# Kernel tuning notes

Hardware: AMD Instinct MI355X
Metric: run time of the kernel (lower is better)

Reference implementation:

```python
import jax, jax.numpy as jnp
import numpy as np

N, M, D = 32768, 2048, 32


def setup_inputs() -> dict:
    key = jax.random.key(0)
    k1, k2, k3, k4 = jax.random.split(key, 4)
    inputs = jax.random.normal(k1, (N, D), dtype=jnp.float32)
    # matches torch init: abs(10*randn*0.1 + 0.2)
    gamma = jnp.abs(10.0 * jax.random.normal(k2, (M, D, D), dtype=jnp.float32) * 0.1 + 0.2)
    means = jax.random.normal(k3, (M, D), dtype=jnp.float32)
    weights = jax.random.normal(k4, (M,), dtype=jnp.float32)
    return {"inputs": inputs, "gamma": gamma, "means": means, "weights": weights}


def reference(inputs, gamma, means, weights):
    # cov_m = gamma_m @ gamma_m^T  -> symmetric PSD [M, D, D]
    cov = jnp.einsum('mde,mfe->mdf', gamma, gamma)
    # Quadratic form (x - mu)^T C (x - mu) expanded (C symmetric):
    # x^T C_m x via GEMM on flattened outer products: [N, D*D] @ [D*D, M]
    xx = (inputs[:, :, None] * inputs[:, None, :]).reshape(inputs.shape[0], -1)
    quad_x = xx @ cov.reshape(cov.shape[0], -1).T            # [N, M]
    b = jnp.einsum('mde,me->md', cov, means)                 # C_m mu_m, [M, D]
    cross = inputs @ b.T                                     # x^T C_m mu_m, [N, M]
    const = jnp.einsum('md,md->m', b, means)                 # mu^T C mu, [M]
    D_ij = quad_x - 2.0 * cross + const[None, :]             # [N, M]
    out = jnp.exp(-D_ij) @ weights                           # [N]
    return out[:, None]
```

## Files before the change

### kernel.cpp

```cpp
#include <hip/hip_runtime.h>
#include <math.h>


#define NN 32768
#define MM 2048
#define DDIM 32
#define KSYM 576
#define ROWS 128
#define KSTEPS 18
#define SCREEN 120.0f
#define MCAP 2048
#define FCAP 1000000
#define FBLK 64

typedef __attribute__((ext_vector_type(8))) short short8;
typedef __attribute__((ext_vector_type(4))) float floatx4;

__device__ __forceinline__ unsigned int to_bf16(float f) {
  union { float f; unsigned int u; } x; x.f = f;
  return (x.u + 0x7fffu + ((x.u >> 16) & 1u)) >> 16;
}

struct DFTab { unsigned char d[528]; unsigned char f[528]; };
constexpr DFTab make_df() {
  DFTab t{};
  int s = 0;
  for (int d = 0; d < 32; ++d)
    for (int f = d; f < 32; ++f) {
      t.d[s] = (unsigned char)d; t.f[s] = (unsigned char)f; ++s;
    }
  return t;
}
constexpr DFTab DFT = make_df();

__device__ __forceinline__ float slot_val(const float* v, int s) {
  if (s < 528) return v[DFT.d[s]] * v[DFT.f[s]];
  if (s < 560) return v[s - 528];
  if (s < 562) return 1.f;
  return 0.f;
}

__device__ __forceinline__ void slot_df(int s, int* dd, int* ff) {
  int d = 0, b = 0;
  while (b + (DDIM - d) <= s) { b += DDIM - d; ++d; }
  *dd = d; *ff = d + (s - b);
}

__global__ __launch_bounds__(256) void build_b_kernel(
    const float* __restrict__ gamma, const float* __restrict__ means,
    unsigned short* __restrict__ Bm, double* __restrict__ acc,
    unsigned int* __restrict__ mcnt, unsigned int* __restrict__ fcount) {
  __shared__ float G[DDIM][DDIM + 1];
  __shared__ float C[DDIM][DDIM + 1];
  __shared__ float bv[DDIM];
  __shared__ float cc;
  const int m = blockIdx.x;
  const int t = threadIdx.x;
  if (t < 16) acc[m * 16 + t] = 0.0;
  if (t == 16) mcnt[m] = 0u;
  if (m == 0 && t == 17) *fcount = 0u;
  const float* g = gamma + (size_t)m * DDIM * DDIM;
  for (int l = t; l < DDIM * DDIM; l += 256) G[l >> 5][l & 31] = g[l];
  __syncthreads();
  const float* mu = means + m * DDIM;
  for (int l = t; l < DDIM * DDIM; l += 256) {
    int d = l >> 5, f = l & 31;
    float c = 0.f;
#pragma unroll
    for (int e = 0; e < DDIM; ++e) c += G[d][e] * G[f][e];
    C[d][f] = c;
  }
  __syncthreads();
  if (t < DDIM) {
    float b = 0.f;
#pragma unroll
    for (int f = 0; f < DDIM; ++f) b += C[t][f] * mu[f];
    bv[t] = b;
  }
  __syncthreads();
  if (t == 0) {
    float c = 0.f;
#pragma unroll
    for (int d = 0; d < DDIM; ++d) c += bv[d] * mu[d];
    cc = c;
  }
  __syncthreads();
  unsigned short* brow = Bm + (size_t)m * KSYM;
  for (int s = t; s < KSYM; s += 256) {
    float val;
    if (s < 528) {
      int d, f; slot_df(s, &d, &f);
      val = (d == f) ? C[d][d] : 2.f * C[d][f];
    } else if (s < 560) {
      val = -2.f * bv[s - 528];
    } else if (s == 560) {
      val = cc;
    } else if (s == 561) {
      unsigned int hi = to_bf16(cc);
      union { unsigned int u; float f; } xh; xh.u = hi << 16;
      val = cc - xh.f;
    } else {
      val = 0.f;
    }
    brow[s] = (unsigned short)to_bf16(val);
  }
}

__device__ __noinline__ double survivor_contrib(
    int m, const float* __restrict__ gamma, const float* __restrict__ means,
    const float* __restrict__ weights, const float* __restrict__ xrow) {
  const float* mu = means + m * DDIM;
  float v[DDIM];
#pragma unroll
  for (int d = 0; d < DDIM; ++d) v[d] = xrow[d] - mu[d];
  const float* g = gamma + (size_t)m * DDIM * DDIM;
  float Dex = 0.f;
  for (int e = 0; e < DDIM; ++e) {
    float y = 0.f;
#pragma unroll
    for (int d = 0; d < DDIM; ++d) y += g[d * DDIM + e] * v[d];
    Dex += y * y;
  }
  float e2 = -Dex * 1.44269504088896340736f;
  float kf = floorf(e2);
  float mant = exp2f(e2 - kf);
  return ldexp((double)(weights[m] * mant), (int)kf);
}

__global__ __launch_bounds__(512, 1) void screen_kernel(
    const float* __restrict__ x, const unsigned short* __restrict__ Bm,
    unsigned int* __restrict__ mcnt, unsigned short* __restrict__ mlist,
    unsigned int* __restrict__ flist, unsigned int* __restrict__ fcount) {
  extern __shared__ __align__(16) unsigned short As[];
  const int t = threadIdx.x;
  const int i0 = blockIdx.x * ROWS;
  const int lane = t & 63, w = t >> 6;
  const int lrow = lane & 15, quad = lane >> 4;
  const int rot = blockIdx.x & 31;

  {
    const int r = t >> 2, j = t & 3;
    float v[DDIM];
#pragma unroll
    for (int q = 0; q < 8; ++q)
      *(floatx4*)&v[q * 4] = *(const floatx4*)(x + (size_t)(i0 + r) * DDIM + q * 4);
#pragma unroll
    for (int jj = 0; jj < 4; ++jj) {
      if (j == jj) {
#pragma unroll
        for (int cc2 = 0; cc2 < 18; ++cc2) {
          const int c = jj * 18 + cc2;
          unsigned int uu[4];
#pragma unroll
          for (int q = 0; q < 4; ++q) {
            const int s0 = c * 8 + q * 2;
            uu[q] = to_bf16(slot_val(v, s0)) | (to_bf16(slot_val(v, s0 + 1)) << 16);
          }
          const int cs = (c & ~7) | ((c & 7) ^ (r & 7));
          uint4 o; o.x = uu[0]; o.y = uu[1]; o.z = uu[2]; o.w = uu[3];
          *(uint4*)&As[r * KSYM + cs * 8] = o;
        }
      }
    }
  }
  __syncthreads();

#pragma unroll 1
  for (int g = 0; g < 4; ++g) {
    const int mq = ((g * 8 + w) + rot) & 31;
    const int m0 = mq * 64;
    const unsigned short* bb0 = Bm + (size_t)(m0 +  0 + lrow) * KSYM + quad * 8;
    const unsigned short* bb1 = Bm + (size_t)(m0 + 16 + lrow) * KSYM + quad * 8;
    const unsigned short* bb2 = Bm + (size_t)(m0 + 32 + lrow) * KSYM + quad * 8;
    const unsigned short* bb3 = Bm + (size_t)(m0 + 48 + lrow) * KSYM + quad * 8;

    floatx4 acc[8][4] = {};
#pragma unroll
    for (int kk = 0; kk < KSTEPS; ++kk) {
      short8 bf[4];
      bf[0] = *(const short8*)(bb0 + kk * 32);
      bf[1] = *(const short8*)(bb1 + kk * 32);
      bf[2] = *(const short8*)(bb2 + kk * 32);
      bf[3] = *(const short8*)(bb3 + kk * 32);
      short8 af[8];
#pragma unroll
      for (int ti = 0; ti < 8; ++ti) {
        int rr = ti * 16 + lrow;
        int c = kk * 4 + quad;
        int cs = (c & ~7) | ((c & 7) ^ (rr & 7));
        af[ti] = *(const short8*)&As[rr * KSYM + cs * 8];
      }
#pragma unroll
      for (int ti = 0; ti < 8; ++ti)
#pragma unroll
        for (int mj = 0; mj < 4; ++mj)
          acc[ti][mj] = __builtin_amdgcn_mfma_f32_16x16x32_bf16(
              af[ti], bf[mj], acc[ti][mj], 0, 0, 0);
    }

#pragma unroll
    for (int ti = 0; ti < 8; ++ti)
#pragma unroll
      for (int mj = 0; mj < 4; ++mj)
#pragma unroll
        for (int r = 0; r < 4; ++r) {
          float Dt = acc[ti][mj][r];
          if (Dt < SCREEN) {
            int gi = i0 + ti * 16 + quad * 4 + r;
            int gm = m0 + mj * 16 + lrow;
            unsigned int idx = atomicAdd(&mcnt[gm], 1u);
            if (idx < MCAP) {
              mlist[(size_t)gm * MCAP + idx] = (unsigned short)gi;
            } else {
              unsigned int fi = atomicAdd(fcount, 1u);
              if (fi < FCAP)
                flist[fi] = ((unsigned int)gi << 11) | (unsigned int)gm;
            }
          }
        }
  }
}

__global__ __launch_bounds__(256) void survivor2_kernel(
    const unsigned int* __restrict__ mcnt, const unsigned short* __restrict__ mlist,
    const unsigned int* __restrict__ flist, const unsigned int* __restrict__ fcount,
    const float* __restrict__ x, const float* __restrict__ gamma,
    const float* __restrict__ means, const float* __restrict__ weights,
    double* __restrict__ acc_out) {
  const int blk = blockIdx.x;
  const int t = threadIdx.x;
  if (blk >= MM) {
    unsigned int total = *fcount;
    if (total > FCAP) total = FCAP;
    for (unsigned int idx = (blk - MM) * 256 + t; idx < total; idx += FBLK * 256) {
      unsigned int p = flist[idx];
      int gi = (int)(p >> 11), gm = (int)(p & 2047u);
      double c = survivor_contrib(gm, gamma, means, weights, x + (size_t)gi * DDIM);
      atomicAdd(&acc_out[gi], c);
    }
    return;
  }
  __shared__ float Gt[DDIM][DDIM + 1];
  __shared__ float mu[DDIM];
  const int m = blk;
  unsigned int cnt = mcnt[m];
  if (cnt > MCAP) cnt = MCAP;
  if (cnt == 0) return;
  const float* g = gamma + (size_t)m * DDIM * DDIM;
  for (int l = t; l < DDIM * DDIM; l += 256) Gt[l & 31][l >> 5] = g[l];
  if (t < DDIM) mu[t] = means[m * DDIM + t];
  __syncthreads();
  const float wm = weights[m];
  for (unsigned int s = t; s < cnt; s += 256) {
    int gi = mlist[(size_t)m * MCAP + s];
    float v[DDIM];
#pragma unroll
    for (int q = 0; q < 8; ++q) {
      floatx4 xv = *(const floatx4*)(x + (size_t)gi * DDIM + q * 4);
      v[q * 4 + 0] = xv.x - mu[q * 4 + 0];
      v[q * 4 + 1] = xv.y - mu[q * 4 + 1];
      v[q * 4 + 2] = xv.z - mu[q * 4 + 2];
      v[q * 4 + 3] = xv.w - mu[q * 4 + 3];
    }
    float Dex = 0.f;
#pragma unroll
    for (int e = 0; e < DDIM; ++e) {
      float y = 0.f;
#pragma unroll
      for (int d = 0; d < DDIM; ++d) y += Gt[e][d] * v[d];
      Dex += y * y;
    }
    float e2 = -Dex * 1.44269504088896340736f;
    float kf = floorf(e2);
    float mant = exp2f(e2 - kf);
    atomicAdd(&acc_out[gi], ldexp((double)(wm * mant), (int)kf));
  }
}

__global__ __launch_bounds__(256) void finalize_kernel(
    const double* __restrict__ acc, float* __restrict__ out) {
  int i = blockIdx.x * 256 + threadIdx.x;
  out[i] = (float)acc[i];
}

extern "C" void kernel_launch(void* const* d_in, const int* in_sizes, int n_in,
                              void* d_out, int out_size, void* d_ws, size_t ws_size,
                              hipStream_t stream) {
  (void)in_sizes; (void)n_in; (void)out_size;
  const float* x       = (const float*)d_in[0];
  const float* gamma   = (const float*)d_in[1];
  const float* means   = (const float*)d_in[2];
  const float* weights = (const float*)d_in[3];

  char* p = (char*)d_ws;
  double* acc          = (double*)p;            p += (size_t)NN * 8;
  unsigned int* fcount = (unsigned int*)p;      p += 16;
  unsigned int* mcnt   = (unsigned int*)p;      p += (size_t)MM * 4;
  unsigned short* mlist= (unsigned short*)p;    p += (size_t)MM * MCAP * 2;
  unsigned int* flist  = (unsigned int*)p;      p += (size_t)FCAP * 4;
  unsigned short* Bm   = (unsigned short*)p;    p += (size_t)MM * KSYM * 2;
  const size_t needed = (size_t)(p - (char*)d_ws);
  if (ws_size < needed) return;

  (void)hipFuncSetAttribute((const void*)screen_kernel,
                            hipFuncAttributeMaxDynamicSharedMemorySize,
                            ROWS * KSYM * 2);

  hipLaunchKernelGGL(build_b_kernel, dim3(MM), dim3(256), 0, stream,
                     gamma, means, Bm, acc, mcnt, fcount);
  hipLaunchKernelGGL(screen_kernel, dim3(NN / ROWS), dim3(512),
                     ROWS * KSYM * 2, stream,
                     x, Bm, mcnt, mlist, flist, fcount);
  hipLaunchKernelGGL(survivor2_kernel, dim3(MM + FBLK), dim3(256), 0, stream,
                     mcnt, mlist, flist, fcount, x, gamma, means, weights, acc);
  hipLaunchKernelGGL(finalize_kernel, dim3(NN / 256), dim3(256), 0, stream,
                     acc, (float*)d_out);
}
```

Before: 182.8 us.

## Precompute bf16 outer-product A matrix in separate kernel; use 16-wave screen blocks

The expansion of each input row into its symmetric outer-product features moves out of the screen kernel into a new agen_kernel that writes them to a global workspace. The screen kernel now copies its 128-row tile straight into shared memory. Blocks grow to 1024 threads, and each wave computes a 64-row by 64-column tile, so the accumulator array halves and register pressure drops. The cost is an extra kernel launch plus a write and re-read of a 32768x576 bf16 buffer through global memory.

```diff
diff --git a/kernel.cpp b/kernel.cpp
--- a/kernel.cpp
+++ b/kernel.cpp
@@ -106,6 +106,31 @@
   }
 }
 
+__global__ __launch_bounds__(256) void agen_kernel(
+    const float* __restrict__ x, unsigned short* __restrict__ Ag) {
+  const int t = threadIdx.x;
+  const int r = blockIdx.x * 32 + (t >> 3);
+  const int j = t & 7;
+  float v[DDIM];
+#pragma unroll
+  for (int q = 0; q < 8; ++q)
+    *(floatx4*)&v[q * 4] = *(const floatx4*)(x + (size_t)r * DDIM + q * 4);
+  unsigned short* arow = Ag + (size_t)r * KSYM;
+#pragma unroll
+  for (int cc2 = 0; cc2 < 9; ++cc2) {
+    const int c = cc2 * 8 + j;
+    unsigned int uu[4];
+#pragma unroll
+    for (int q = 0; q < 4; ++q) {
+      const int s0 = c * 8 + q * 2;
+      uu[q] = to_bf16(slot_val(v, s0)) | (to_bf16(slot_val(v, s0 + 1)) << 16);
+    }
+    const int cs = (c & ~7) | ((c & 7) ^ (r & 7));
+    uint4 o; o.x = uu[0]; o.y = uu[1]; o.z = uu[2]; o.w = uu[3];
+    *(uint4*)&arow[cs * 8] = o;
+  }
+}
+
 __device__ __noinline__ double survivor_contrib(
     int m, const float* __restrict__ gamma, const float* __restrict__ means,
     const float* __restrict__ weights, const float* __restrict__ xrow) {
@@ -127,8 +152,10 @@
   return ldexp((double)(weights[m] * mant), (int)kf);
 }
 
-__global__ __launch_bounds__(512, 1) void screen_kernel(
-    const float* __restrict__ x, const unsigned short* __restrict__ Bm,
+__global__ __launch_bounds__(1024)
+__attribute__((amdgpu_waves_per_eu(4, 4)))
+void screen_kernel(
+    const unsigned short* __restrict__ Ag, const unsigned short* __restrict__ Bm,
     unsigned int* __restrict__ mcnt, unsigned short* __restrict__ mlist,
     unsigned int* __restrict__ flist, unsigned int* __restrict__ fcount) {
   extern __shared__ __align__(16) unsigned short As[];
@@ -139,42 +166,26 @@
   const int rot = blockIdx.x & 31;
 
   {
-    const int r = t >> 2, j = t & 3;
-    float v[DDIM];
-#pragma unroll
-    for (int q = 0; q < 8; ++q)
-      *(floatx4*)&v[q * 4] = *(const floatx4*)(x + (size_t)(i0 + r) * DDIM + q * 4);
-#pragma unroll
-    for (int jj = 0; jj < 4; ++jj) {
-      if (j == jj) {
-#pragma unroll
-        for (int cc2 = 0; cc2 < 18; ++cc2) {
-          const int c = jj * 18 + cc2;
-          unsigned int uu[4];
-#pragma unroll
-          for (int q = 0; q < 4; ++q) {
-            const int s0 = c * 8 + q * 2;
-            uu[q] = to_bf16(slot_val(v, s0)) | (to_bf16(slot_val(v, s0 + 1)) << 16);
-          }
-          const int cs = (c & ~7) | ((c & 7) ^ (r & 7));
-          uint4 o; o.x = uu[0]; o.y = uu[1]; o.z = uu[2]; o.w = uu[3];
-          *(uint4*)&As[r * KSYM + cs * 8] = o;
-        }
-      }
-    }
+    const uint4* __restrict__ src = (const uint4*)(Ag + (size_t)i0 * KSYM);
+    uint4* __restrict__ dst = (uint4*)As;
+#pragma unroll
+    for (int ofs = 0; ofs < 9; ++ofs)
+      dst[ofs * 1024 + t] = src[ofs * 1024 + t];
   }
   __syncthreads();
 
 #pragma unroll 1
   for (int g = 0; g < 4; ++g) {
-    const int mq = ((g * 8 + w) + rot) & 31;
-    const int m0 = mq * 64;
+    const int task = g * 16 + w;
+    const int rh = task >> 5;
+    const int cg = ((task & 31) + rot) & 31;
+    const int m0 = cg * 64;
     const unsigned short* bb0 = Bm + (size_t)(m0 +  0 + lrow) * KSYM + quad * 8;
     const unsigned short* bb1 = Bm + (size_t)(m0 + 16 + lrow) * KSYM + quad * 8;
     const unsigned short* bb2 = Bm + (size_t)(m0 + 32 + lrow) * KSYM + quad * 8;
     const unsigned short* bb3 = Bm + (size_t)(m0 + 48 + lrow) * KSYM + quad * 8;
 
-    floatx4 acc[8][4] = {};
+    floatx4 acc[4][4] = {};
 #pragma unroll
     for (int kk = 0; kk < KSTEPS; ++kk) {
       short8 bf[4];
@@ -182,31 +193,28 @@
       bf[1] = *(const short8*)(bb1 + kk * 32);
       bf[2] = *(const short8*)(bb2 + kk * 32);
       bf[3] = *(const short8*)(bb3 + kk * 32);
-      short8 af[8];
-#pragma unroll
-      for (int ti = 0; ti < 8; ++ti) {
-        int rr = ti * 16 + lrow;
-        int c = kk * 4 + quad;
-        int cs = (c & ~7) | ((c & 7) ^ (rr & 7));
-        af[ti] = *(const short8*)&As[rr * KSYM + cs * 8];
-      }
-#pragma unroll
-      for (int ti = 0; ti < 8; ++ti)
+#pragma unroll
+      for (int ti = 0; ti < 4; ++ti) {
+        const int rr = rh * 64 + ti * 16 + lrow;
+        const int c = kk * 4 + quad;
+        const int cs = (c & ~7) | ((c & 7) ^ (rr & 7));
+        short8 a = *(const short8*)&As[rr * KSYM + cs * 8];
 #pragma unroll
         for (int mj = 0; mj < 4; ++mj)
           acc[ti][mj] = __builtin_amdgcn_mfma_f32_16x16x32_bf16(
-              af[ti], bf[mj], acc[ti][mj], 0, 0, 0);
-    }
-
-#pragma unroll
-    for (int ti = 0; ti < 8; ++ti)
+              a, bf[mj], acc[ti][mj], 0, 0, 0);
+      }
+    }
+
+#pragma unroll
+    for (int ti = 0; ti < 4; ++ti)
 #pragma unroll
       for (int mj = 0; mj < 4; ++mj)
 #pragma unroll
         for (int r = 0; r < 4; ++r) {
           float Dt = acc[ti][mj][r];
           if (Dt < SCREEN) {
-            int gi = i0 + ti * 16 + quad * 4 + r;
+            int gi = i0 + rh * 64 + ti * 16 + quad * 4 + r;
             int gm = m0 + mj * 16 + lrow;
             unsigned int idx = atomicAdd(&mcnt[gm], 1u);
             if (idx < MCAP) {
@@ -299,6 +307,7 @@
   unsigned short* mlist= (unsigned short*)p;    p += (size_t)MM * MCAP * 2;
   unsigned int* flist  = (unsigned int*)p;      p += (size_t)FCAP * 4;
   unsigned short* Bm   = (unsigned short*)p;    p += (size_t)MM * KSYM * 2;
+  unsigned short* Ag   = (unsigned short*)p;    p += (size_t)NN * KSYM * 2;
   const size_t needed = (size_t)(p - (char*)d_ws);
   if (ws_size < needed) return;
 
@@ -308,9 +317,11 @@
 
   hipLaunchKernelGGL(build_b_kernel, dim3(MM), dim3(256), 0, stream,
                      gamma, means, Bm, acc, mcnt, fcount);
-  hipLaunchKernelGGL(screen_kernel, dim3(NN / ROWS), dim3(512),
+  hipLaunchKernelGGL(agen_kernel, dim3(NN / 32), dim3(256), 0, stream,
+                     x, Ag);
+  hipLaunchKernelGGL(screen_kernel, dim3(NN / ROWS), dim3(1024),
                      ROWS * KSYM * 2, stream,
-                     x, Bm, mcnt, mlist, flist, fcount);
+                     Ag, Bm, mcnt, mlist, flist, fcount);
   hipLaunchKernelGGL(survivor2_kernel, dim3(MM + FBLK), dim3(256), 0, stream,
                      mcnt, mlist, flist, fcount, x, gamma, means, weights, acc);
   hipLaunchKernelGGL(finalize_kernel, dim3(NN / 256), dim3(256), 0, stream,
```

Result: slower. 307.0 us (+67.9%).

## Precompute swizzled bf16 outer-product rows in prep kernel and stream into LDS

Applied to the files above, without the earlier changes.

The per-row symmetric outer-product expansion and bf16 packing moves out of the screen kernel into extra blocks of the prep kernel, which write a pre-swizzled global buffer Ag. The screen kernel now copies that buffer straight into shared memory with wide loads, instead of computing it with a thread layout where only a quarter of the lanes were active at a time. The A-fragment LDS addresses are also precomputed per tile row to cut address arithmetic in the MFMA inner loop. The cost is an extra 36 MB global write and read round trip plus a larger workspace.

```diff
diff --git a/kernel.cpp b/kernel.cpp
--- a/kernel.cpp
+++ b/kernel.cpp
@@ -46,16 +46,41 @@
   *dd = d; *ff = d + (s - b);
 }
 
-__global__ __launch_bounds__(256) void build_b_kernel(
+__global__ __launch_bounds__(256) void prep_kernel(
     const float* __restrict__ gamma, const float* __restrict__ means,
     unsigned short* __restrict__ Bm, double* __restrict__ acc,
-    unsigned int* __restrict__ mcnt, unsigned int* __restrict__ fcount) {
+    unsigned int* __restrict__ mcnt, unsigned int* __restrict__ fcount,
+    const float* __restrict__ x, unsigned short* __restrict__ Ag) {
+  const int t = threadIdx.x;
+  if (blockIdx.x >= MM) {
+    const int blk = blockIdx.x - MM;
+    const int r = blk * 32 + (t >> 3);
+    const int j = t & 7;
+    float v[DDIM];
+#pragma unroll
+    for (int q = 0; q < 8; ++q)
+      *(floatx4*)&v[q * 4] = *(const floatx4*)(x + (size_t)r * DDIM + q * 4);
+    unsigned short* arow = Ag + (size_t)r * KSYM;
+#pragma unroll
+    for (int cc2 = 0; cc2 < 9; ++cc2) {
+      const int c = cc2 * 8 + j;
+      unsigned int uu[4];
+#pragma unroll
+      for (int q = 0; q < 4; ++q) {
+        const int s0 = c * 8 + q * 2;
+        uu[q] = to_bf16(slot_val(v, s0)) | (to_bf16(slot_val(v, s0 + 1)) << 16);
+      }
+      const int cs = (c & ~7) | ((c & 7) ^ (r & 7));
+      uint4 o; o.x = uu[0]; o.y = uu[1]; o.z = uu[2]; o.w = uu[3];
+      *(uint4*)&arow[cs * 8] = o;
+    }
+    return;
+  }
   __shared__ float G[DDIM][DDIM + 1];
   __shared__ float C[DDIM][DDIM + 1];
   __shared__ float bv[DDIM];
   __shared__ float cc;
   const int m = blockIdx.x;
-  const int t = threadIdx.x;
   if (t < 16) acc[m * 16 + t] = 0.0;
   if (t == 16) mcnt[m] = 0u;
   if (m == 0 && t == 17) *fcount = 0u;
@@ -128,7 +153,7 @@
 }
 
 __global__ __launch_bounds__(512, 1) void screen_kernel(
-    const float* __restrict__ x, const unsigned short* __restrict__ Bm,
+    const unsigned short* __restrict__ Ag, const unsigned short* __restrict__ Bm,
     unsigned int* __restrict__ mcnt, unsigned short* __restrict__ mlist,
     unsigned int* __restrict__ flist, unsigned int* __restrict__ fcount) {
   extern __shared__ __align__(16) unsigned short As[];
@@ -139,31 +164,23 @@
   const int rot = blockIdx.x & 31;
 
   {
-    const int r = t >> 2, j = t & 3;
-    float v[DDIM];
-#pragma unroll
-    for (int q = 0; q < 8; ++q)
-      *(floatx4*)&v[q * 4] = *(const floatx4*)(x + (size_t)(i0 + r) * DDIM + q * 4);
-#pragma unroll
-    for (int jj = 0; jj < 4; ++jj) {
-      if (j == jj) {
-#pragma unroll
-        for (int cc2 = 0; cc2 < 18; ++cc2) {
-          const int c = jj * 18 + cc2;
-          unsigned int uu[4];
-#pragma unroll
-          for (int q = 0; q < 4; ++q) {
-            const int s0 = c * 8 + q * 2;
-            uu[q] = to_bf16(slot_val(v, s0)) | (to_bf16(slot_val(v, s0 + 1)) << 16);
-          }
-          const int cs = (c & ~7) | ((c & 7) ^ (r & 7));
-          uint4 o; o.x = uu[0]; o.y = uu[1]; o.z = uu[2]; o.w = uu[3];
-          *(uint4*)&As[r * KSYM + cs * 8] = o;
-        }
-      }
-    }
-  }
-  __syncthreads();
+    const uint4* __restrict__ src = (const uint4*)(Ag + (size_t)i0 * KSYM);
+    uint4* __restrict__ dst = (uint4*)As;
+#pragma unroll
+    for (int ofs = 0; ofs < 18; ++ofs)
+      dst[ofs * 512 + t] = src[ofs * 512 + t];
+  }
+  __syncthreads();
+
+  const char* pae[8];
+  const char* pao[8];
+#pragma unroll
+  for (int ti = 0; ti < 8; ++ti) {
+    const int rr = ti * 16 + lrow;
+    const char* rowb = (const char*)As + rr * (KSYM * 2);
+    pae[ti] = rowb + 16 * (quad ^ (rr & 7));
+    pao[ti] = rowb + 16 * ((4 | quad) ^ (rr & 7));
+  }
 
 #pragma unroll 1
   for (int g = 0; g < 4; ++g) {
@@ -182,20 +199,15 @@
       bf[1] = *(const short8*)(bb1 + kk * 32);
       bf[2] = *(const short8*)(bb2 + kk * 32);
       bf[3] = *(const short8*)(bb3 + kk * 32);
-      short8 af[8];
 #pragma unroll
       for (int ti = 0; ti < 8; ++ti) {
-        int rr = ti * 16 + lrow;
-        int c = kk * 4 + quad;
-        int cs = (c & ~7) | ((c & 7) ^ (rr & 7));
-        af[ti] = *(const short8*)&As[rr * KSYM + cs * 8];
-      }
-#pragma unroll
-      for (int ti = 0; ti < 8; ++ti)
+        const char* pa = (kk & 1) ? pao[ti] : pae[ti];
+        short8 a = *(const short8*)(pa + (kk >> 1) * 128);
 #pragma unroll
         for (int mj = 0; mj < 4; ++mj)
           acc[ti][mj] = __builtin_amdgcn_mfma_f32_16x16x32_bf16(
-              af[ti], bf[mj], acc[ti][mj], 0, 0, 0);
+              a, bf[mj], acc[ti][mj], 0, 0, 0);
+      }
     }
 
 #pragma unroll
@@ -299,6 +311,7 @@
   unsigned short* mlist= (unsigned short*)p;    p += (size_t)MM * MCAP * 2;
   unsigned int* flist  = (unsigned int*)p;      p += (size_t)FCAP * 4;
   unsigned short* Bm   = (unsigned short*)p;    p += (size_t)MM * KSYM * 2;
+  unsigned short* Ag   = (unsigned short*)p;    p += (size_t)NN * KSYM * 2;
   const size_t needed = (size_t)(p - (char*)d_ws);
   if (ws_size < needed) return;
 
@@ -306,11 +319,11 @@
                             hipFuncAttributeMaxDynamicSharedMemorySize,
                             ROWS * KSYM * 2);
 
-  hipLaunchKernelGGL(build_b_kernel, dim3(MM), dim3(256), 0, stream,
-                     gamma, means, Bm, acc, mcnt, fcount);
+  hipLaunchKernelGGL(prep_kernel, dim3(MM + NN / 32), dim3(256), 0, stream,
+                     gamma, means, Bm, acc, mcnt, fcount, x, Ag);
   hipLaunchKernelGGL(screen_kernel, dim3(NN / ROWS), dim3(512),
                      ROWS * KSYM * 2, stream,
-                     x, Bm, mcnt, mlist, flist, fcount);
+                     Ag, Bm, mcnt, mlist, flist, fcount);
   hipLaunchKernelGGL(survivor2_kernel, dim3(MM + FBLK), dim3(256), 0, stream,
                      mcnt, mlist, flist, fcount, x, gamma, means, weights, acc);
   hipLaunchKernelGGL(finalize_kernel, dim3(NN / 256), dim3(256), 0, stream,
```

Result: slower. 257.5 us (+40.8%).
